# Kernel optimization log

Measured on AMD Instinct MI355X. Metric: run time of the kernel, lower is better.

Reference implementation:

```python
import jax, jax.numpy as jnp
import numpy as np


def setup_inputs() -> dict:
    key = jax.random.key(0)
    D = 4096
    B = 4096
    # State vector stacked as (2*D, B); original torch code uses complex64 but
    # all operator entries sqrt(i+1) are real, so float32 computes identical values.
    x = jax.random.normal(key, (2 * D, B), dtype=jnp.float32)
    return {"x": x}


def reference(x):
    # y = (U kron I2) @ x where U[i, i+1] = sqrt(i+1) (annihilation operator).
    # Row r = 2*i + j of the kron operator picks x[2*(i+1) + j] * sqrt(i+1),
    # and the last row-pair (i = D-1) is zero. Implemented as a shift-and-scale
    # over adjacent row pairs -- same math as the dense matmul, no D^2 kron.
    twoD, B = x.shape
    D = twoD // 2
    xr = x.reshape(D, 2, B)                                   # (D, 2, B)
    coef = jnp.sqrt(jnp.arange(1, D, dtype=x.dtype))          # sqrt(1..D-1)
    y = jnp.concatenate(
        [coef[:, None, None] * xr[1:], jnp.zeros_like(xr[:1])], axis=0
    )                                                         # (D, 2, B)
    return y.reshape(twoD, B)
```

## Files before the change

### kernel.cpp

```cpp
#include <hip/hip_runtime.h>


typedef float vf4 __attribute__((ext_vector_type(4)));

constexpr int kD = 4096;
constexpr int kB = 4096;
constexpr int kV4Row  = kB / 4;
constexpr int kV4Pair = 2 * kV4Row;
constexpr int kPT     = 8;

__global__ __launch_bounds__(256) void destroy_kernel(
    const vf4* __restrict__ x, vf4* __restrict__ y) {
    const int t  = threadIdx.x;
    const int pA = blockIdx.x * 2;
    const int pB = pA + 1;

    const int baseA = pA * kV4Pair + t;
    const int baseB = pB * kV4Pair + t;

    const bool  lastB = (pB == kD - 1);
    const float cA = sqrtf((float)(pA + 1));
    const float cB = lastB ? 0.f : sqrtf((float)(pB + 1));
    const int   srcB = lastB ? baseB : (baseB + kV4Pair);

    vf4 va[kPT], vb[kPT];
#pragma unroll
    for (int j = 0; j < kPT; ++j)
        va[j] = x[baseA + kV4Pair + j * 256];
#pragma unroll
    for (int j = 0; j < kPT; ++j)
        vb[j] = x[srcB + j * 256];

#pragma unroll
    for (int j = 0; j < kPT; ++j)
        y[baseA + j * 256] = cA * va[j];
#pragma unroll
    for (int j = 0; j < kPT; ++j)
        y[baseB + j * 256] = cB * vb[j];
}

extern "C" void kernel_launch(void* const* d_in, const int* in_sizes, int n_in,
                              void* d_out, int out_size, void* d_ws, size_t ws_size,
                              hipStream_t stream) {
    const vf4* x = (const vf4*)d_in[0];
    vf4* y = (vf4*)d_out;
    destroy_kernel<<<dim3(kD / 2), dim3(256), 0, stream>>>(x, y);
}
```

Baseline: 232.8 us.

## Process four strided row-pairs per block with nontemporal loads and stores

Cuts the grid from 2048 to 1024 blocks, each handling four row-pairs spaced kBlocks apart. Loads and stores are interleaved in a software-pipelined order with double buffers, and all memory accesses use nontemporal hints so the streaming copy bypasses cache retention. The aim is more bytes in flight per thread and less cache pollution, at the cost of fewer waves and more registers per thread.

```diff
diff --git a/kernel.cpp b/kernel.cpp
--- a/kernel.cpp
+++ b/kernel.cpp
@@ -8,35 +8,62 @@
 constexpr int kV4Row  = kB / 4;
 constexpr int kV4Pair = 2 * kV4Row;
 constexpr int kPT     = 8;
+constexpr int kBlocks = 1024;
 
 __global__ __launch_bounds__(256) void destroy_kernel(
     const vf4* __restrict__ x, vf4* __restrict__ y) {
-    const int t  = threadIdx.x;
-    const int pA = blockIdx.x * 2;
-    const int pB = pA + 1;
+    const int t = threadIdx.x;
 
-    const int baseA = pA * kV4Pair + t;
-    const int baseB = pB * kV4Pair + t;
+    const int p0 = blockIdx.x;
+    const int p1 = p0 + kBlocks;
+    const int p2 = p0 + 2 * kBlocks;
+    const int p3 = p0 + 3 * kBlocks;
 
-    const bool  lastB = (pB == kD - 1);
-    const float cA = sqrtf((float)(pA + 1));
-    const float cB = lastB ? 0.f : sqrtf((float)(pB + 1));
-    const int   srcB = lastB ? baseB : (baseB + kV4Pair);
+    const int  s0 = (p0 + 1) * kV4Pair + t;
+    const int  s1 = (p1 + 1) * kV4Pair + t;
+    const int  s2 = (p2 + 1) * kV4Pair + t;
+    const bool last3 = (p3 == kD - 1);
+    const int  s3 = (last3 ? p3 : p3 + 1) * kV4Pair + t;
 
-    vf4 va[kPT], vb[kPT];
-#pragma unroll
-    for (int j = 0; j < kPT; ++j)
-        va[j] = x[baseA + kV4Pair + j * 256];
-#pragma unroll
-    for (int j = 0; j < kPT; ++j)
-        vb[j] = x[srcB + j * 256];
+    const int  d0 = p0 * kV4Pair + t;
+    const int  d1 = p1 * kV4Pair + t;
+    const int  d2 = p2 * kV4Pair + t;
+    const int  d3 = p3 * kV4Pair + t;
+
+    const float c0 = sqrtf((float)(p0 + 1));
+    const float c1 = sqrtf((float)(p1 + 1));
+    const float c2 = sqrtf((float)(p2 + 1));
+    const float c3 = last3 ? 0.f : sqrtf((float)(p3 + 1));
+
+    vf4 a[kPT], b[kPT];
 
 #pragma unroll
     for (int j = 0; j < kPT; ++j)
-        y[baseA + j * 256] = cA * va[j];
+        a[j] = __builtin_nontemporal_load(&x[s0 + j * 256]);
 #pragma unroll
     for (int j = 0; j < kPT; ++j)
-        y[baseB + j * 256] = cB * vb[j];
+        b[j] = __builtin_nontemporal_load(&x[s1 + j * 256]);
+
+#pragma unroll
+    for (int j = 0; j < kPT; ++j)
+        __builtin_nontemporal_store(c0 * a[j], &y[d0 + j * 256]);
+#pragma unroll
+    for (int j = 0; j < kPT; ++j)
+        a[j] = __builtin_nontemporal_load(&x[s2 + j * 256]);
+
+#pragma unroll
+    for (int j = 0; j < kPT; ++j)
+        __builtin_nontemporal_store(c1 * b[j], &y[d1 + j * 256]);
+#pragma unroll
+    for (int j = 0; j < kPT; ++j)
+        b[j] = __builtin_nontemporal_load(&x[s3 + j * 256]);
+
+#pragma unroll
+    for (int j = 0; j < kPT; ++j)
+        __builtin_nontemporal_store(c2 * a[j], &y[d2 + j * 256]);
+#pragma unroll
+    for (int j = 0; j < kPT; ++j)
+        __builtin_nontemporal_store(c3 * b[j], &y[d3 + j * 256]);
 }
 
 extern "C" void kernel_launch(void* const* d_in, const int* in_sizes, int n_in,
@@ -44,5 +71,5 @@
                               hipStream_t stream) {
     const vf4* x = (const vf4*)d_in[0];
     vf4* y = (vf4*)d_out;
-    destroy_kernel<<<dim3(kD / 2), dim3(256), 0, stream>>>(x, y);
+    destroy_kernel<<<dim3(kBlocks), dim3(256), 0, stream>>>(x, y);
 }
```

Measured after the change: 218.2 us. -6.2%, faster.
